# Optimization experiments

Hardware: AMD Instinct MI355X
Metric: run time of the kernel (lower is better)

Reference implementation:

```python
import jax, jax.numpy as jnp
import numpy as np

DIM = 4096
N_HEADS = 32
N_KV_HEADS = 8
HEAD_DIM = DIM // N_HEADS            # 128
GROUP = N_HEADS // N_KV_HEADS        # 4 heads share each kv head


def setup_inputs() -> dict:
    key = jax.random.key(0)
    k1, k2, k3, k4 = jax.random.split(key, 4)
    B, S = 2, 2048
    x = jax.random.normal(k1, (B, S, DIM), dtype=jnp.float32)
    # nn.Linear weights are [out_features, in_features]
    Wq = jax.random.normal(k2, (N_HEADS * HEAD_DIM, DIM), dtype=jnp.float32) * 0.02
    Wkv = jax.random.normal(k3, (2 * N_KV_HEADS * HEAD_DIM, DIM), dtype=jnp.float32) * 0.02
    Wo = jax.random.normal(k4, (DIM, N_HEADS * HEAD_DIM), dtype=jnp.float32) * 0.02
    return {"x": x, "Wq": Wq, "Wkv": Wkv, "Wo": Wo, "start_pos": 0}


def reference(x, Wq, Wkv, Wo, start_pos):
    B, S, _ = x.shape
    total_len = start_pos + S
    # projections (Linear: x @ W.T)
    q = (x @ Wq.T).reshape(B, S, N_HEADS, HEAD_DIM)                  # (B,S,H,D)
    kv = (x @ Wkv.T).reshape(B, S, 2 * N_KV_HEADS, HEAD_DIM)
    k, v = jnp.split(kv, 2, axis=2)                                   # (B,S,Hkv,D) each
    # cache write + read with start_pos=0 is identity on k, v (prefill)
    # inflate kv heads: repeat_interleave along head axis
    k = jnp.repeat(k, GROUP, axis=2)                                  # (B,T,H,D)
    v = jnp.repeat(v, GROUP, axis=2)
    scale = HEAD_DIM ** -0.5
    scores = jnp.einsum('bqhd,bkhd->bhqk', q, k) * scale              # (B,H,S,T)
    q_idx = jnp.arange(total_len - S, total_len)[:, None]
    k_idx = jnp.arange(total_len)[None, :]
    causal = q_idx >= k_idx                                           # (S,T)
    scores = jnp.where(causal[None, None], scores, -jnp.inf)
    probs = jax.nn.softmax(scores, axis=-1)
    attn = jnp.einsum('bhqk,bkhd->bqhd', probs, v)                    # (B,S,H,D)
    attn = attn.reshape(B, S, N_HEADS * HEAD_DIM)
    return attn @ Wo.T                                                # (B,S,dim)
```

## Files before the change

kernel.cpp:

```cpp
#include <hip/hip_runtime.h>

typedef __bf16 bf16x8 __attribute__((ext_vector_type(8)));
typedef __bf16 bf16x4 __attribute__((ext_vector_type(4)));
typedef float f32x4 __attribute__((ext_vector_type(4)));
typedef unsigned short u16;
typedef unsigned short u16x8 __attribute__((ext_vector_type(8)));

#define DIM 4096
#define NHEADS 32
#define NKV 8
#define HD 128
#define BB 2
#define SS 2048
#define MROWS (BB*SS)
#define QKVP 6144
#define QSCALE 0.08838834764831843f

#define WAIT_LGKM0 asm volatile("s_waitcnt lgkmcnt(0)" ::: "memory")
#define WAIT_VM0   asm volatile("s_waitcnt vmcnt(0)" ::: "memory")
#define WAIT_VM4   asm volatile("s_waitcnt vmcnt(4)" ::: "memory")
#define WAIT_VM8   asm volatile("s_waitcnt vmcnt(8)" ::: "memory")
#define SGB0       __builtin_amdgcn_sched_barrier(0)

__device__ __forceinline__ u16 f2bf(float f) {
  unsigned int u = __float_as_uint(f);
  u += 0x7fffu + ((u >> 16) & 1u);
  return (u16)(u >> 16);
}

__device__ __forceinline__ void gload16(const void* g, void* l) {
  __builtin_amdgcn_global_load_lds(
      (const __attribute__((address_space(1))) unsigned int*)g,
      (__attribute__((address_space(3))) unsigned int*)l, 16, 0, 0);
}

__device__ __forceinline__ bf16x4 tr16(const void* p) {
  bf16x4 d;
  asm volatile("ds_read_b64_tr_b16 %0, %1"
               : "=v"(d)
               : "v"((const __attribute__((address_space(3))) u16*)p)
               : "memory");
  return d;
}

template<int CTRL>
__device__ __forceinline__ float dpp_ror(float x) {
  return __int_as_float(__builtin_amdgcn_update_dpp(
      0, __float_as_int(x), CTRL, 0xF, 0xF, false));
}
__device__ __forceinline__ float red16_max(float v) {
  v = fmaxf(v, dpp_ror<0x121>(v));
  v = fmaxf(v, dpp_ror<0x122>(v));
  v = fmaxf(v, dpp_ror<0x124>(v));
  v = fmaxf(v, dpp_ror<0x128>(v));
  return v;
}
__device__ __forceinline__ float red16_sum(float v) {
  v += dpp_ror<0x121>(v);
  v += dpp_ror<0x122>(v);
  v += dpp_ror<0x124>(v);
  v += dpp_ror<0x128>(v);
  return v;
}

__global__ __launch_bounds__(256) void f2b_kernel(const float* __restrict__ in,
                                                  u16* __restrict__ out, int n8) {
  int i = blockIdx.x * 256 + threadIdx.x;
  if (i >= n8) return;
  const float4* in4 = (const float4*)in;
  float4 a = in4[2*(size_t)i];
  float4 b = in4[2*(size_t)i + 1];
  u16x8 o;
  o[0]=f2bf(a.x); o[1]=f2bf(a.y); o[2]=f2bf(a.z); o[3]=f2bf(a.w);
  o[4]=f2bf(b.x); o[5]=f2bf(b.y); o[6]=f2bf(b.z); o[7]=f2bf(b.w);
  ((u16x8*)out)[i] = o;
}

template<int OUTF32>
__global__ __launch_bounds__(512, 2) void gemm256(
    const u16* __restrict__ A, const u16* __restrict__ Bm, void* __restrict__ C,
    int M, int N, int K, int nbx, int acut, float a0, float a1) {
  __shared__ char smem[131072];

  const int t = threadIdx.x;
  const int l = t & 63, w = t >> 6;
  const int l15 = l & 15, l4 = l >> 4;
  const int wm = w >> 2, wn = w & 3;

  const int nwg = gridDim.x;
  const int cpx = nwg >> 3;
  const int sw = (blockIdx.x & 7) * cpx + (blockIdx.x >> 3);
  const int bx = sw % nbx, by = sw / nbx;
  const int row0 = by * 256, col0 = bx * 256;
  const float alpha = (col0 < acut) ? a0 : a1;

  f32x4 acc[8][4] = {};

  auto stage = [&](int kt) {
    const int bsel = kt & 3;
    const int k0 = kt << 5;
    char* Ad = smem + bsel * 16384;
    char* Bd = smem + 65536 + bsel * 16384;
    #pragma unroll
    for (int i = 0; i < 2; ++i) {
      int o = (i*8 + w)*64 + l;
      int j = o >> 3;
      int cs = (o & 7) ^ (j & 7);
      int r = 2*j + (cs >> 2);
      int kc = (cs & 3) * 8;
      gload16((const char*)A + ((size_t)(row0 + r)*K + k0 + kc)*2,
              Ad + (i*8 + w)*1024);
      gload16((const char*)Bm + ((size_t)(col0 + r)*K + k0 + kc)*2,
              Bd + (i*8 + w)*1024);
    }
  };

  const int nt = K >> 5;
  stage(0); stage(1); stage(2);
  WAIT_VM8;
  __builtin_amdgcn_s_barrier();
  SGB0;

  for (int kt = 0; kt < nt; ++kt) {
    if (kt + 3 < nt) { stage(kt + 3); WAIT_VM8; }
    else if (kt + 2 < nt) { WAIT_VM4; }
    else if (kt + 1 < nt) { WAIT_VM0; }
    __builtin_amdgcn_s_barrier();
    SGB0;

    const char* Ab = smem + (kt & 3) * 16384;
    const char* Bb = smem + 65536 + (kt & 3) * 16384;
    bf16x8 af[8], bfv[4];
    #pragma unroll
    for (int mi = 0; mi < 8; ++mi) {
      int r = wm*128 + mi*16 + l15;
      int j = r >> 1;
      int c = ((r & 1)*4 + l4) ^ (j & 7);
      af[mi] = *(const bf16x8*)(Ab + j*128 + c*16);
    }
    #pragma unroll
    for (int ni = 0; ni < 4; ++ni) {
      int r = wn*64 + ni*16 + l15;
      int j = r >> 1;
      int c = ((r & 1)*4 + l4) ^ (j & 7);
      bfv[ni] = *(const bf16x8*)(Bb + j*128 + c*16);
    }
    __builtin_amdgcn_s_setprio(1);
    #pragma unroll
    for (int mi = 0; mi < 8; ++mi)
      #pragma unroll
      for (int ni = 0; ni < 4; ++ni)
        acc[mi][ni] = __builtin_amdgcn_mfma_f32_16x16x32_bf16(
            af[mi], bfv[ni], acc[mi][ni], 0, 0, 0);
    __builtin_amdgcn_s_setprio(0);
    SGB0;
    __builtin_amdgcn_s_barrier();
    SGB0;
  }

  #pragma unroll
  for (int mi = 0; mi < 8; ++mi) {
    #pragma unroll
    for (int ni = 0; ni < 4; ++ni) {
      #pragma unroll
      for (int r = 0; r < 4; ++r) {
        size_t rr = (size_t)(row0 + wm*128 + mi*16 + l4*4 + r);
        size_t cc = (size_t)(col0 + wn*64 + ni*16 + l15);
        float v = acc[mi][ni][r] * alpha;
        if (OUTF32) ((float*)C)[rr*(size_t)N + cc] = v;
        else        ((u16*)C)[rr*(size_t)N + cc] = f2bf(v);
      }
    }
  }
}

__global__ __launch_bounds__(256, 2) void attn_kernel(
    const u16* __restrict__ QKV,
    u16* __restrict__ O) {
  __shared__ u16 Ks[2][64*128];
  __shared__ u16 Vs[2][64*128];
  __shared__ u16 Ps[4][1024];
  const int t = threadIdx.x;
  const int l = t & 63, w = t >> 6;
  const int l15 = l & 15, l4 = l >> 4;
  const int pair = blockIdx.x, h = blockIdx.y, b = blockIdx.z;
  const int hkv = h >> 2;
  const u16* Kg = QKV + (size_t)(b*SS) * QKVP + DIM + hkv*HD;
  const u16* Vg = Kg + NKV*HD;
  u16* Pw = &Ps[w][0];

  auto stage = [&](u16* Ksb, u16* Vsb, int kv0) {
    const u16* Kr = Kg + (size_t)kv0 * QKVP;
    const u16* Vr = Vg + (size_t)kv0 * QKVP;
    #pragma unroll
    for (int i = 0; i < 4; ++i) {
      int o = i*4096 + w*1024 + l*16;
      int row = o >> 8;
      int sc = l15 ^ (row & 7);
      gload16((const char*)(Kr + (size_t)row * QKVP) + sc*16,
              (char*)Ksb + i*4096 + w*1024);
    }
    #pragma unroll
    for (int i = 0; i < 4; ++i) {
      int cb = i*4 + w;
      int kv = cb*4 + ((l & 7) >> 1);
      int d0 = ((l >> 3) << 4) + (l & 1)*8;
      gload16((const char*)(Vr + (size_t)kv * QKVP + d0),
              (char*)Vsb + cb*1024);
    }
  };

  for (int half = 0; half < 2; ++half) {
    const int qb = half ? (15 - pair) : pair;
    const int q0 = qb * 128;
    const int q0w = q0 + w*32;

    const size_t qbase = ((size_t)(b*SS + q0w)) * QKVP + h*HD;
    bf16x8 qf[2][4];
    #pragma unroll
    for (int m = 0; m < 2; ++m)
      #pragma unroll
      for (int kd = 0; kd < 4; ++kd)
        qf[m][kd] = *(const bf16x8*)&QKV[qbase + (size_t)(m*16 + l15)*QKVP + kd*32 + l4*8];

    f32x4 oacc[2][8] = {};
    float mrun[2][4], lrun[2][4];
    #pragma unroll
    for (int m = 0; m < 2; ++m)
      #pragma unroll
      for (int r = 0; r < 4; ++r) { mrun[m][r] = -1e30f; lrun[m][r] = 0.f; }

    const int nst = 2*qb + 2;
    stage(Ks[0], Vs[0], 0);
    WAIT_VM0;
    __builtin_amdgcn_s_barrier();
    SGB0;

    for (int st = 0; st < nst; ++st) {
      const int kv0 = st * 64;
      u16* Ksb = Ks[st & 1];
      u16* Vsb = Vs[st & 1];
      if (st + 1 < nst) stage(Ks[(st+1) & 1], Vs[(st+1) & 1], kv0 + 64);

      if (kv0 <= q0w + 31) {
        f32x4 sacc[2][4] = {};
        __builtin_amdgcn_s_setprio(1);
        #pragma unroll
        for (int kd = 0; kd < 4; ++kd) {
          bf16x8 kf[4];
          #pragma unroll
          for (int n = 0; n < 4; ++n) {
            int row = n*16 + l15;
            int off = (row << 8) | (((kd*4 + l4) ^ (row & 7)) << 4);
            kf[n] = *(const bf16x8*)((const char*)Ksb + off);
          }
          #pragma unroll
          for (int m = 0; m < 2; ++m)
            #pragma unroll
            for (int n = 0; n < 4; ++n)
              sacc[m][n] = __builtin_amdgcn_mfma_f32_16x16x32_bf16(qf[m][kd], kf[n], sacc[m][n], 0, 0, 0);
        }
        __builtin_amdgcn_s_setprio(0);

        if (st >= 2*qb) {
          #pragma unroll
          for (int n = 0; n < 4; ++n) {
            int ki = kv0 + n*16 + l15;
            #pragma unroll
            for (int m = 0; m < 2; ++m)
              #pragma unroll
              for (int r = 0; r < 4; ++r) {
                int qi = q0w + m*16 + l4*4 + r;
                if (ki > qi) sacc[m][n][r] = -1e30f;
              }
          }
        }

        float pr[2][4][4];
        #pragma unroll
        for (int m = 0; m < 2; ++m) {
          #pragma unroll
          for (int r = 0; r < 4; ++r) {
            float s0 = sacc[m][0][r], s1 = sacc[m][1][r];
            float s2 = sacc[m][2][r], s3 = sacc[m][3][r];
            float vm = fmaxf(fmaxf(s0, s1), fmaxf(s2, s3));
            vm = red16_max(vm);
            float mo = mrun[m][r];
            float mnew = fmaxf(mo, vm);
            float al = __expf(mo - mnew);
            float p0 = __expf(s0 - mnew), p1 = __expf(s1 - mnew);
            float p2 = __expf(s2 - mnew), p3 = __expf(s3 - mnew);
            float rs = red16_sum((p0 + p1) + (p2 + p3));
            mrun[m][r] = mnew;
            lrun[m][r] = lrun[m][r]*al + rs;
            #pragma unroll
            for (int dn = 0; dn < 8; ++dn) oacc[m][dn][r] *= al;
            pr[m][r][0] = p0; pr[m][r][1] = p1; pr[m][r][2] = p2; pr[m][r][3] = p3;
          }
        }

        #pragma unroll
        for (int kvh = 0; kvh < 2; ++kvh) {
          #pragma unroll
          for (int m = 0; m < 2; ++m)
            #pragma unroll
            for (int nn = 0; nn < 2; ++nn) {
              int n = kvh*2 + nn;
              bf16x4 w4;
              w4[0] = (__bf16)pr[m][0][n]; w4[1] = (__bf16)pr[m][1][n];
              w4[2] = (__bf16)pr[m][2][n]; w4[3] = (__bf16)pr[m][3][n];
              *(bf16x4*)((char*)Pw + ((nn*4 + (l15 >> 2))*2 + m)*128
                                   + (l15 & 3)*32 + l4*8) = w4;
            }
          const char* pb = (const char*)Pw + l4*512 + l15*8;
          bf16x4 a00 = tr16(pb);
          bf16x4 a01 = tr16(pb + 256);
          bf16x4 a10 = tr16(pb + 128);
          bf16x4 a11 = tr16(pb + 384);
          const char* vb = (const char*)Vsb + l4*2048 + l15*8 + kvh*8192;
          bf16x4 b0[8], b1[8];
          #pragma unroll
          for (int dn = 0; dn < 8; ++dn) {
            b0[dn] = tr16(vb + dn*128);
            b1[dn] = tr16(vb + dn*128 + 1024);
          }
          WAIT_LGKM0; SGB0;
          bf16x8 pa0 = __builtin_shufflevector(a00, a01, 0,1,2,3,4,5,6,7);
          bf16x8 pa1 = __builtin_shufflevector(a10, a11, 0,1,2,3,4,5,6,7);
          __builtin_amdgcn_s_setprio(1);
          #pragma unroll
          for (int dn = 0; dn < 8; ++dn) {
            bf16x8 v8 = __builtin_shufflevector(b0[dn], b1[dn], 0,1,2,3,4,5,6,7);
            oacc[0][dn] = __builtin_amdgcn_mfma_f32_16x16x32_bf16(pa0, v8, oacc[0][dn], 0, 0, 0);
            oacc[1][dn] = __builtin_amdgcn_mfma_f32_16x16x32_bf16(pa1, v8, oacc[1][dn], 0, 0, 0);
          }
          __builtin_amdgcn_s_setprio(0);
        }
      }

      WAIT_VM0;
      __builtin_amdgcn_s_barrier();
      SGB0;
    }

    const size_t obase = ((size_t)(b*SS + q0w)) * DIM + h*HD;
    #pragma unroll
    for (int m = 0; m < 2; ++m) {
      #pragma unroll
      for (int r = 0; r < 4; ++r) {
        float inv = 1.0f / lrun[m][r];
        int srow = m*16 + l4*4 + r;
        #pragma unroll
        for (int dn = 0; dn < 8; ++dn)
          O[obase + (size_t)srow*DIM + dn*16 + l15] = f2bf(oacc[m][dn][r] * inv);
      }
    }
  }
}

extern "C" void kernel_launch(void* const* d_in, const int* in_sizes, int n_in,
                              void* d_out, int out_size, void* d_ws, size_t ws_size,
                              hipStream_t stream) {
  const float* x   = (const float*)d_in[0];
  const float* Wq  = (const float*)d_in[1];
  const float* Wkv = (const float*)d_in[2];
  const float* Wo  = (const float*)d_in[3];

  if (ws_size < (160ull << 20)) return;
  char* ws = (char*)d_ws;
  u16* xb   = (u16*)(ws);
  u16* Wqb  = (u16*)(ws + (32ull  << 20));
  u16* Wkvb = (u16*)(ws + (64ull  << 20));
  u16* Wob  = (u16*)(ws + (80ull  << 20));
  u16* QKVb = (u16*)(ws + (112ull << 20));
  u16* attnb = xb;

  f2b_kernel<<<8192, 256, 0, stream>>>(x,   xb,   2097152);
  f2b_kernel<<<8192, 256, 0, stream>>>(Wq,  Wqb,  2097152);
  f2b_kernel<<<4096, 256, 0, stream>>>(Wkv, Wkvb, 1048576);
  f2b_kernel<<<8192, 256, 0, stream>>>(Wo,  Wob,  2097152);

  gemm256<0><<<dim3(16*24), 512, 0, stream>>>(xb, Wqb, QKVb,
                                              MROWS, QKVP, DIM, 24, DIM, QSCALE, 1.0f);

  attn_kernel<<<dim3(8, NHEADS, BB), 256, 0, stream>>>(QKVb, attnb);

  gemm256<1><<<dim3(16*16), 512, 0, stream>>>(attnb, Wob, d_out,
                                              MROWS, DIM, DIM, 16, 0, 1.0f, 1.0f);
}
```

Before: 571.4 us.

## Split GEMM main loop into two MFMA phases interleaved with A/B prefetch

Restructures the bf16 GEMM K-loop so each iteration runs two halves of MFMAs (rows 0-3, then 4-7). The global prefetch of the A tile is issued during the first half and the B tile during the second, with barriers and priority hints between them. The vmcnt wait moves to the end of the iteration so loads for the next tile overlap compute. The aim is to hide global-load and LDS-read latency behind MFMA work and to lower fragment register pressure. The cost is extra barriers per iteration, which could add synchronization stalls.

```diff
diff --git a/kernel.cpp b/kernel.cpp
--- a/kernel.cpp
+++ b/kernel.cpp
@@ -96,11 +96,10 @@
 
   f32x4 acc[8][4] = {};
 
-  auto stage = [&](int kt) {
+  auto stageM = [&](const u16* Mp, int base0, int kt) {
     const int bsel = kt & 3;
     const int k0 = kt << 5;
-    char* Ad = smem + bsel * 16384;
-    char* Bd = smem + 65536 + bsel * 16384;
+    char* Md = smem + base0 + bsel * 16384;
     #pragma unroll
     for (int i = 0; i < 2; ++i) {
       int o = (i*8 + w)*64 + l;
@@ -108,54 +107,89 @@
       int cs = (o & 7) ^ (j & 7);
       int r = 2*j + (cs >> 2);
       int kc = (cs & 3) * 8;
-      gload16((const char*)A + ((size_t)(row0 + r)*K + k0 + kc)*2,
-              Ad + (i*8 + w)*1024);
-      gload16((const char*)Bm + ((size_t)(col0 + r)*K + k0 + kc)*2,
-              Bd + (i*8 + w)*1024);
+      gload16((const char*)Mp + ((size_t)(base0 ? col0 + r : row0 + r)*K + k0 + kc)*2,
+              Md + (i*8 + w)*1024);
     }
   };
 
+  auto ldA = [&](const char* Ab, int mi) -> bf16x8 {
+    int r = wm*128 + mi*16 + l15;
+    int j = r >> 1;
+    int c = ((r & 1)*4 + l4) ^ (j & 7);
+    return *(const bf16x8*)(Ab + j*128 + c*16);
+  };
+  auto ldB = [&](const char* Bb, int ni) -> bf16x8 {
+    int r = wn*64 + ni*16 + l15;
+    int j = r >> 1;
+    int c = ((r & 1)*4 + l4) ^ (j & 7);
+    return *(const bf16x8*)(Bb + j*128 + c*16);
+  };
+
   const int nt = K >> 5;
-  stage(0); stage(1); stage(2);
+  stageM(A, 0, 0); stageM(Bm, 65536, 0);
+  stageM(A, 0, 1); stageM(Bm, 65536, 1);
+  stageM(A, 0, 2); stageM(Bm, 65536, 2);
   WAIT_VM8;
   __builtin_amdgcn_s_barrier();
-  SGB0;
 
   for (int kt = 0; kt < nt; ++kt) {
-    if (kt + 3 < nt) { stage(kt + 3); WAIT_VM8; }
-    else if (kt + 2 < nt) { WAIT_VM4; }
-    else if (kt + 1 < nt) { WAIT_VM0; }
-    __builtin_amdgcn_s_barrier();
-    SGB0;
-
     const char* Ab = smem + (kt & 3) * 16384;
     const char* Bb = smem + 65536 + (kt & 3) * 16384;
-    bf16x8 af[8], bfv[4];
-    #pragma unroll
-    for (int mi = 0; mi < 8; ++mi) {
-      int r = wm*128 + mi*16 + l15;
-      int j = r >> 1;
-      int c = ((r & 1)*4 + l4) ^ (j & 7);
-      af[mi] = *(const bf16x8*)(Ab + j*128 + c*16);
-    }
-    #pragma unroll
-    for (int ni = 0; ni < 4; ++ni) {
-      int r = wn*64 + ni*16 + l15;
-      int j = r >> 1;
-      int c = ((r & 1)*4 + l4) ^ (j & 7);
-      bfv[ni] = *(const bf16x8*)(Bb + j*128 + c*16);
-    }
+    const bool pf = (kt + 3 < nt);
+
+    bf16x8 af0 = ldA(Ab, 0), af1 = ldA(Ab, 1), af2 = ldA(Ab, 2), af3 = ldA(Ab, 3);
+    bf16x8 bf0 = ldB(Bb, 0), bf1 = ldB(Bb, 1), bf2 = ldB(Bb, 2), bf3 = ldB(Bb, 3);
+    SGB0;
+    if (pf) stageM(A, 0, kt + 3);
+    __builtin_amdgcn_s_barrier();
+    WAIT_LGKM0; SGB0;
     __builtin_amdgcn_s_setprio(1);
-    #pragma unroll
-    for (int mi = 0; mi < 8; ++mi)
-      #pragma unroll
-      for (int ni = 0; ni < 4; ++ni)
-        acc[mi][ni] = __builtin_amdgcn_mfma_f32_16x16x32_bf16(
-            af[mi], bfv[ni], acc[mi][ni], 0, 0, 0);
+    acc[0][0] = __builtin_amdgcn_mfma_f32_16x16x32_bf16(af0, bf0, acc[0][0], 0, 0, 0);
+    acc[0][1] = __builtin_amdgcn_mfma_f32_16x16x32_bf16(af0, bf1, acc[0][1], 0, 0, 0);
+    acc[0][2] = __builtin_amdgcn_mfma_f32_16x16x32_bf16(af0, bf2, acc[0][2], 0, 0, 0);
+    acc[0][3] = __builtin_amdgcn_mfma_f32_16x16x32_bf16(af0, bf3, acc[0][3], 0, 0, 0);
+    acc[1][0] = __builtin_amdgcn_mfma_f32_16x16x32_bf16(af1, bf0, acc[1][0], 0, 0, 0);
+    acc[1][1] = __builtin_amdgcn_mfma_f32_16x16x32_bf16(af1, bf1, acc[1][1], 0, 0, 0);
+    acc[1][2] = __builtin_amdgcn_mfma_f32_16x16x32_bf16(af1, bf2, acc[1][2], 0, 0, 0);
+    acc[1][3] = __builtin_amdgcn_mfma_f32_16x16x32_bf16(af1, bf3, acc[1][3], 0, 0, 0);
+    acc[2][0] = __builtin_amdgcn_mfma_f32_16x16x32_bf16(af2, bf0, acc[2][0], 0, 0, 0);
+    acc[2][1] = __builtin_amdgcn_mfma_f32_16x16x32_bf16(af2, bf1, acc[2][1], 0, 0, 0);
+    acc[2][2] = __builtin_amdgcn_mfma_f32_16x16x32_bf16(af2, bf2, acc[2][2], 0, 0, 0);
+    acc[2][3] = __builtin_amdgcn_mfma_f32_16x16x32_bf16(af2, bf3, acc[2][3], 0, 0, 0);
+    acc[3][0] = __builtin_amdgcn_mfma_f32_16x16x32_bf16(af3, bf0, acc[3][0], 0, 0, 0);
+    acc[3][1] = __builtin_amdgcn_mfma_f32_16x16x32_bf16(af3, bf1, acc[3][1], 0, 0, 0);
+    acc[3][2] = __builtin_amdgcn_mfma_f32_16x16x32_bf16(af3, bf2, acc[3][2], 0, 0, 0);
+    acc[3][3] = __builtin_amdgcn_mfma_f32_16x16x32_bf16(af3, bf3, acc[3][3], 0, 0, 0);
     __builtin_amdgcn_s_setprio(0);
+    __builtin_amdgcn_s_barrier();
+
+    bf16x8 af4 = ldA(Ab, 4), af5 = ldA(Ab, 5), af6 = ldA(Ab, 6), af7 = ldA(Ab, 7);
     SGB0;
+    if (pf) stageM(Bm, 65536, kt + 3);
     __builtin_amdgcn_s_barrier();
-    SGB0;
+    WAIT_LGKM0; SGB0;
+    __builtin_amdgcn_s_setprio(1);
+    acc[4][0] = __builtin_amdgcn_mfma_f32_16x16x32_bf16(af4, bf0, acc[4][0], 0, 0, 0);
+    acc[4][1] = __builtin_amdgcn_mfma_f32_16x16x32_bf16(af4, bf1, acc[4][1], 0, 0, 0);
+    acc[4][2] = __builtin_amdgcn_mfma_f32_16x16x32_bf16(af4, bf2, acc[4][2], 0, 0, 0);
+    acc[4][3] = __builtin_amdgcn_mfma_f32_16x16x32_bf16(af4, bf3, acc[4][3], 0, 0, 0);
+    acc[5][0] = __builtin_amdgcn_mfma_f32_16x16x32_bf16(af5, bf0, acc[5][0], 0, 0, 0);
+    acc[5][1] = __builtin_amdgcn_mfma_f32_16x16x32_bf16(af5, bf1, acc[5][1], 0, 0, 0);
+    acc[5][2] = __builtin_amdgcn_mfma_f32_16x16x32_bf16(af5, bf2, acc[5][2], 0, 0, 0);
+    acc[5][3] = __builtin_amdgcn_mfma_f32_16x16x32_bf16(af5, bf3, acc[5][3], 0, 0, 0);
+    acc[6][0] = __builtin_amdgcn_mfma_f32_16x16x32_bf16(af6, bf0, acc[6][0], 0, 0, 0);
+    acc[6][1] = __builtin_amdgcn_mfma_f32_16x16x32_bf16(af6, bf1, acc[6][1], 0, 0, 0);
+    acc[6][2] = __builtin_amdgcn_mfma_f32_16x16x32_bf16(af6, bf2, acc[6][2], 0, 0, 0);
+    acc[6][3] = __builtin_amdgcn_mfma_f32_16x16x32_bf16(af6, bf3, acc[6][3], 0, 0, 0);
+    acc[7][0] = __builtin_amdgcn_mfma_f32_16x16x32_bf16(af7, bf0, acc[7][0], 0, 0, 0);
+    acc[7][1] = __builtin_amdgcn_mfma_f32_16x16x32_bf16(af7, bf1, acc[7][1], 0, 0, 0);
+    acc[7][2] = __builtin_amdgcn_mfma_f32_16x16x32_bf16(af7, bf2, acc[7][2], 0, 0, 0);
+    acc[7][3] = __builtin_amdgcn_mfma_f32_16x16x32_bf16(af7, bf3, acc[7][3], 0, 0, 0);
+    __builtin_amdgcn_s_setprio(0);
+    if (pf)                { WAIT_VM8; }
+    else if (kt + 2 < nt)  { WAIT_VM4; }
+    else if (kt + 1 < nt)  { WAIT_VM0; }
+    __builtin_amdgcn_s_barrier();
   }
 
   #pragma unroll
```

Result: no change. 564.5 us (-1.2%).

## Software-pipeline GEMM LDS fragment loads and merge four conversion kernels

Applied to the files above, without the earlier changes.

The GEMM main loop is unrolled by two with ping-pong register fragment sets. Each iteration issues the LDS reads for the next k-tile while the MFMAs for the current tile run, and keeps one barrier per tile instead of two. Global load addresses are precomputed once and advanced by pointer increments, which removes the per-stage index math. The four fp32-to-bf16 conversion launches are merged into a single launch. The risks are higher register pressure from holding two fragment sets and a tighter WAR margin on the four-buffer LDS ring.

```diff
diff --git a/kernel.cpp b/kernel.cpp
--- a/kernel.cpp
+++ b/kernel.cpp
@@ -19,7 +19,6 @@
 #define WAIT_LGKM0 asm volatile("s_waitcnt lgkmcnt(0)" ::: "memory")
 #define WAIT_VM0   asm volatile("s_waitcnt vmcnt(0)" ::: "memory")
 #define WAIT_VM4   asm volatile("s_waitcnt vmcnt(4)" ::: "memory")
-#define WAIT_VM8   asm volatile("s_waitcnt vmcnt(8)" ::: "memory")
 #define SGB0       __builtin_amdgcn_sched_barrier(0)
 
 __device__ __forceinline__ u16 f2bf(float f) {
@@ -63,17 +62,24 @@
   return v;
 }
 
-__global__ __launch_bounds__(256) void f2b_kernel(const float* __restrict__ in,
-                                                  u16* __restrict__ out, int n8) {
+__global__ __launch_bounds__(256) void f2b4_kernel(
+    const float* __restrict__ xa, const float* __restrict__ xb,
+    const float* __restrict__ xc, const float* __restrict__ xd,
+    u16* __restrict__ oa, u16* __restrict__ ob,
+    u16* __restrict__ oc, u16* __restrict__ od) {
   int i = blockIdx.x * 256 + threadIdx.x;
-  if (i >= n8) return;
+  const float* in; u16* out; int k;
+  if (i < 2097152)      { in = xa; out = oa; k = i; }
+  else if (i < 4194304) { in = xb; out = ob; k = i - 2097152; }
+  else if (i < 5242880) { in = xc; out = oc; k = i - 4194304; }
+  else                  { in = xd; out = od; k = i - 5242880; }
   const float4* in4 = (const float4*)in;
-  float4 a = in4[2*(size_t)i];
-  float4 b = in4[2*(size_t)i + 1];
+  float4 a = in4[2*(size_t)k];
+  float4 b = in4[2*(size_t)k + 1];
   u16x8 o;
   o[0]=f2bf(a.x); o[1]=f2bf(a.y); o[2]=f2bf(a.z); o[3]=f2bf(a.w);
   o[4]=f2bf(b.x); o[5]=f2bf(b.y); o[6]=f2bf(b.z); o[7]=f2bf(b.w);
-  ((u16x8*)out)[i] = o;
+  ((u16x8*)out)[k] = o;
 }
 
 template<int OUTF32>
@@ -96,66 +102,127 @@
 
   f32x4 acc[8][4] = {};
 
-  auto stage = [&](int kt) {
-    const int bsel = kt & 3;
-    const int k0 = kt << 5;
-    char* Ad = smem + bsel * 16384;
-    char* Bd = smem + 65536 + bsel * 16384;
-    #pragma unroll
-    for (int i = 0; i < 2; ++i) {
-      int o = (i*8 + w)*64 + l;
-      int j = o >> 3;
-      int cs = (o & 7) ^ (j & 7);
-      int r = 2*j + (cs >> 2);
-      int kc = (cs & 3) * 8;
-      gload16((const char*)A + ((size_t)(row0 + r)*K + k0 + kc)*2,
-              Ad + (i*8 + w)*1024);
-      gload16((const char*)Bm + ((size_t)(col0 + r)*K + k0 + kc)*2,
-              Bd + (i*8 + w)*1024);
-    }
+  int ro0, ko0, ro1, ko1;
+  {
+    int o = t, j = o >> 3, cs = (o & 7) ^ (j & 7);
+    ro0 = 2*j + (cs >> 2); ko0 = (cs & 3) * 8;
+    o = t + 512; j = o >> 3; cs = (o & 7) ^ (j & 7);
+    ro1 = 2*j + (cs >> 2); ko1 = (cs & 3) * 8;
+  }
+  const char* gA0 = (const char*)(A  + (size_t)(row0 + ro0) * K + ko0);
+  const char* gA1 = (const char*)(A  + (size_t)(row0 + ro1) * K + ko1);
+  const char* gB0 = (const char*)(Bm + (size_t)(col0 + ro0) * K + ko0);
+  const char* gB1 = (const char*)(Bm + (size_t)(col0 + ro1) * K + ko1);
+
+  auto stage = [&](int bsel) {
+    char* Ad = (char*)smem + bsel * 16384;
+    char* Bd = Ad + 65536;
+    gload16(gA0, Ad + w*1024);
+    gload16(gA1, Ad + 8192 + w*1024);
+    gload16(gB0, Bd + w*1024);
+    gload16(gB1, Bd + 8192 + w*1024);
+    gA0 += 64; gA1 += 64; gB0 += 64; gB1 += 64;
   };
 
+  int offA0, offB0;
+  {
+    int r = wm*128 + l15, j = r >> 1;
+    int c = ((r & 1)*4 + l4) ^ (j & 7);
+    offA0 = j*128 + c*16;
+    r = wn*64 + l15; j = r >> 1;
+    c = ((r & 1)*4 + l4) ^ (j & 7);
+    offB0 = 65536 + j*128 + c*16;
+  }
+
+  struct Frags { bf16x8 a0,a1,a2,a3,a4,a5,a6,a7,b0,b1,b2,b3; };
+  Frags F0, F1;
+
+  auto loadF = [&](Frags& F, int bsel) {
+    const char* Sb = (const char*)smem + bsel * 16384;
+    const char* Ab = Sb + offA0;
+    const char* Bb = Sb + offB0;
+    F.a0 = *(const bf16x8*)(Ab);
+    F.a1 = *(const bf16x8*)(Ab + 1024);
+    F.a2 = *(const bf16x8*)(Ab + 2048);
+    F.a3 = *(const bf16x8*)(Ab + 3072);
+    F.a4 = *(const bf16x8*)(Ab + 4096);
+    F.a5 = *(const bf16x8*)(Ab + 5120);
+    F.a6 = *(const bf16x8*)(Ab + 6144);
+    F.a7 = *(const bf16x8*)(Ab + 7168);
+    F.b0 = *(const bf16x8*)(Bb);
+    F.b1 = *(const bf16x8*)(Bb + 1024);
+    F.b2 = *(const bf16x8*)(Bb + 2048);
+    F.b3 = *(const bf16x8*)(Bb + 3072);
+  };
+
+  auto mfmaC = [&](const Frags& F) {
+    __builtin_amdgcn_s_setprio(1);
+    acc[0][0] = __builtin_amdgcn_mfma_f32_16x16x32_bf16(F.a0, F.b0, acc[0][0], 0, 0, 0);
+    acc[0][1] = __builtin_amdgcn_mfma_f32_16x16x32_bf16(F.a0, F.b1, acc[0][1], 0, 0, 0);
+    acc[0][2] = __builtin_amdgcn_mfma_f32_16x16x32_bf16(F.a0, F.b2, acc[0][2], 0, 0, 0);
+    acc[0][3] = __builtin_amdgcn_mfma_f32_16x16x32_bf16(F.a0, F.b3, acc[0][3], 0, 0, 0);
+    acc[1][0] = __builtin_amdgcn_mfma_f32_16x16x32_bf16(F.a1, F.b0, acc[1][0], 0, 0, 0);
+    acc[1][1] = __builtin_amdgcn_mfma_f32_16x16x32_bf16(F.a1, F.b1, acc[1][1], 0, 0, 0);
+    acc[1][2] = __builtin_amdgcn_mfma_f32_16x16x32_bf16(F.a1, F.b2, acc[1][2], 0, 0, 0);
+    acc[1][3] = __builtin_amdgcn_mfma_f32_16x16x32_bf16(F.a1, F.b3, acc[1][3], 0, 0, 0);
+    acc[2][0] = __builtin_amdgcn_mfma_f32_16x16x32_bf16(F.a2, F.b0, acc[2][0], 0, 0, 0);
+    acc[2][1] = __builtin_amdgcn_mfma_f32_16x16x32_bf16(F.a2, F.b1, acc[2][1], 0, 0, 0);
+    acc[2][2] = __builtin_amdgcn_mfma_f32_16x16x32_bf16(F.a2, F.b2, acc[2][2], 0, 0, 0);
+    acc[2][3] = __builtin_amdgcn_mfma_f32_16x16x32_bf16(F.a2, F.b3, acc[2][3], 0, 0, 0);
+    acc[3][0] = __builtin_amdgcn_mfma_f32_16x16x32_bf16(F.a3, F.b0, acc[3][0], 0, 0, 0);
+    acc[3][1] = __builtin_amdgcn_mfma_f32_16x16x32_bf16(F.a3, F.b1, acc[3][1], 0, 0, 0);
+    acc[3][2] = __builtin_amdgcn_mfma_f32_16x16x32_bf16(F.a3, F.b2, acc[3][2], 0, 0, 0);
+    acc[3][3] = __builtin_amdgcn_mfma_f32_16x16x32_bf16(F.a3, F.b3, acc[3][3], 0, 0, 0);
+    acc[4][0] = __builtin_amdgcn_mfma_f32_16x16x32_bf16(F.a4, F.b0, acc[4][0], 0, 0, 0);
+    acc[4][1] = __builtin_amdgcn_mfma_f32_16x16x32_bf16(F.a4, F.b1, acc[4][1], 0, 0, 0);
+    acc[4][2] = __builtin_amdgcn_mfma_f32_16x16x32_bf16(F.a4, F.b2, acc[4][2], 0, 0, 0);
+    acc[4][3] = __builtin_amdgcn_mfma_f32_16x16x32_bf16(F.a4, F.b3, acc[4][3], 0, 0, 0);
+    acc[5][0] = __builtin_amdgcn_mfma_f32_16x16x32_bf16(F.a5, F.b0, acc[5][0], 0, 0, 0);
+    acc[5][1] = __builtin_amdgcn_mfma_f32_16x16x32_bf16(F.a5, F.b1, acc[5][1], 0, 0, 0);
+    acc[5][2] = __builtin_amdgcn_mfma_f32_16x16x32_bf16(F.a5, F.b2, acc[5][2], 0, 0, 0);
+    acc[5][3] = __builtin_amdgcn_mfma_f32_16x16x32_bf16(F.a5, F.b3, acc[5][3], 0, 0, 0);
+    acc[6][0] = __builtin_amdgcn_mfma_f32_16x16x32_bf16(F.a6, F.b0, acc[6][0], 0, 0, 0);
+    acc[6][1] = __builtin_amdgcn_mfma_f32_16x16x32_bf16(F.a6, F.b1, acc[6][1], 0, 0, 0);
+    acc[6][2] = __builtin_amdgcn_mfma_f32_16x16x32_bf16(F.a6, F.b2, acc[6][2], 0, 0, 0);
+    acc[6][3] = __builtin_amdgcn_mfma_f32_16x16x32_bf16(F.a6, F.b3, acc[6][3], 0, 0, 0);
+    acc[7][0] = __builtin_amdgcn_mfma_f32_16x16x32_bf16(F.a7, F.b0, acc[7][0], 0, 0, 0);
+    acc[7][1] = __builtin_amdgcn_mfma_f32_16x16x32_bf16(F.a7, F.b1, acc[7][1], 0, 0, 0);
+    acc[7][2] = __builtin_amdgcn_mfma_f32_16x16x32_bf16(F.a7, F.b2, acc[7][2], 0, 0, 0);
+    acc[7][3] = __builtin_amdgcn_mfma_f32_16x16x32_bf16(F.a7, F.b3, acc[7][3], 0, 0, 0);
+    __builtin_amdgcn_s_setprio(0);
+  };
+
   const int nt = K >> 5;
+
   stage(0); stage(1); stage(2);
-  WAIT_VM8;
+  WAIT_VM4;
   __builtin_amdgcn_s_barrier();
-  SGB0;
-
-  for (int kt = 0; kt < nt; ++kt) {
-    if (kt + 3 < nt) { stage(kt + 3); WAIT_VM8; }
-    else if (kt + 2 < nt) { WAIT_VM4; }
-    else if (kt + 1 < nt) { WAIT_VM0; }
-    __builtin_amdgcn_s_barrier();
-    SGB0;
-
-    const char* Ab = smem + (kt & 3) * 16384;
-    const char* Bb = smem + 65536 + (kt & 3) * 16384;
-    bf16x8 af[8], bfv[4];
-    #pragma unroll
-    for (int mi = 0; mi < 8; ++mi) {
-      int r = wm*128 + mi*16 + l15;
-      int j = r >> 1;
-      int c = ((r & 1)*4 + l4) ^ (j & 7);
-      af[mi] = *(const bf16x8*)(Ab + j*128 + c*16);
-    }
-    #pragma unroll
-    for (int ni = 0; ni < 4; ++ni) {
-      int r = wn*64 + ni*16 + l15;
-      int j = r >> 1;
-      int c = ((r & 1)*4 + l4) ^ (j & 7);
-      bfv[ni] = *(const bf16x8*)(Bb + j*128 + c*16);
-    }
-    __builtin_amdgcn_s_setprio(1);
-    #pragma unroll
-    for (int mi = 0; mi < 8; ++mi)
-      #pragma unroll
-      for (int ni = 0; ni < 4; ++ni)
-        acc[mi][ni] = __builtin_amdgcn_mfma_f32_16x16x32_bf16(
-            af[mi], bfv[ni], acc[mi][ni], 0, 0, 0);
-    __builtin_amdgcn_s_setprio(0);
-    SGB0;
-    __builtin_amdgcn_s_barrier();
-    SGB0;
+  loadF(F0, 0);
+  WAIT_LGKM0; SGB0;
+
+  for (int i = 0; i < nt; i += 2) {
+    {
+      const bool pf = (i + 3 < nt);
+      if (pf) stage((i + 3) & 3);
+      if (i + 1 < nt) loadF(F1, (i + 1) & 3);
+      SGB0;
+      mfmaC(F0);
+      SGB0;
+      WAIT_LGKM0; SGB0;
+      if (pf) { WAIT_VM4; } else { WAIT_VM0; }
+      __builtin_amdgcn_s_barrier();
+    }
+    if (i + 1 < nt) {
+      const bool pf = (i + 4 < nt);
+      if (pf) stage((i + 4) & 3);
+      if (i + 2 < nt) loadF(F0, (i + 2) & 3);
+      SGB0;
+      mfmaC(F1);
+      SGB0;
+      WAIT_LGKM0; SGB0;
+      if (pf) { WAIT_VM4; } else { WAIT_VM0; }
+      __builtin_amdgcn_s_barrier();
+    }
   }
 
   #pragma unroll
@@ -375,10 +442,7 @@
   u16* QKVb = (u16*)(ws + (112ull << 20));
   u16* attnb = xb;
 
-  f2b_kernel<<<8192, 256, 0, stream>>>(x,   xb,   2097152);
-  f2b_kernel<<<8192, 256, 0, stream>>>(Wq,  Wqb,  2097152);
-  f2b_kernel<<<4096, 256, 0, stream>>>(Wkv, Wkvb, 1048576);
-  f2b_kernel<<<8192, 256, 0, stream>>>(Wo,  Wob,  2097152);
+  f2b4_kernel<<<28672, 256, 0, stream>>>(x, Wq, Wkv, Wo, xb, Wqb, Wkvb, Wob);
 
   gemm256<0><<<dim3(16*24), 512, 0, stream>>>(xb, Wqb, QKVb,
                                               MROWS, QKVP, DIM, 24, DIM, QSCALE, 1.0f);
```

New measurement: 543.6 us. -4.9%, faster.

## Load GEMM B operand directly to registers and fuse the four bf16 conversion launches

Applied to the files above, without the earlier changes.

The GEMM mainloop now stages only the A tile through LDS, double-buffered with a K-step of 64, and reads the B operand straight from global memory into registers. This halves LDS use and removes the LDS reads for B, but each wave now issues its own B global loads and the pipeline is shallower (2 buffers instead of 4). The four fp32-to-bf16 conversion launches are also merged into one kernel that picks its source by index range, cutting launch overhead.

```diff
diff --git a/kernel.cpp b/kernel.cpp
--- a/kernel.cpp
+++ b/kernel.cpp
@@ -63,24 +63,31 @@
   return v;
 }
 
-__global__ __launch_bounds__(256) void f2b_kernel(const float* __restrict__ in,
-                                                  u16* __restrict__ out, int n8) {
+__global__ __launch_bounds__(256) void f2b4_kernel(
+    const float* __restrict__ xa, const float* __restrict__ xb,
+    const float* __restrict__ xc, const float* __restrict__ xd,
+    u16* __restrict__ oa, u16* __restrict__ ob,
+    u16* __restrict__ oc, u16* __restrict__ od) {
   int i = blockIdx.x * 256 + threadIdx.x;
-  if (i >= n8) return;
+  const float* in; u16* out; int k;
+  if (i < 2097152)      { in = xa; out = oa; k = i; }
+  else if (i < 4194304) { in = xb; out = ob; k = i - 2097152; }
+  else if (i < 5242880) { in = xc; out = oc; k = i - 4194304; }
+  else                  { in = xd; out = od; k = i - 5242880; }
   const float4* in4 = (const float4*)in;
-  float4 a = in4[2*(size_t)i];
-  float4 b = in4[2*(size_t)i + 1];
+  float4 a = in4[2*(size_t)k];
+  float4 b = in4[2*(size_t)k + 1];
   u16x8 o;
   o[0]=f2bf(a.x); o[1]=f2bf(a.y); o[2]=f2bf(a.z); o[3]=f2bf(a.w);
   o[4]=f2bf(b.x); o[5]=f2bf(b.y); o[6]=f2bf(b.z); o[7]=f2bf(b.w);
-  ((u16x8*)out)[i] = o;
+  ((u16x8*)out)[k] = o;
 }
 
 template<int OUTF32>
 __global__ __launch_bounds__(512, 2) void gemm256(
     const u16* __restrict__ A, const u16* __restrict__ Bm, void* __restrict__ C,
     int M, int N, int K, int nbx, int acut, float a0, float a1) {
-  __shared__ char smem[131072];
+  __shared__ char smem[65536];
 
   const int t = threadIdx.x;
   const int l = t & 63, w = t >> 6;
@@ -96,67 +103,81 @@
 
   f32x4 acc[8][4] = {};
 
-  auto stage = [&](int kt) {
-    const int bsel = kt & 3;
-    const int k0 = kt << 5;
-    char* Ad = smem + bsel * 16384;
-    char* Bd = smem + 65536 + bsel * 16384;
-    #pragma unroll
-    for (int i = 0; i < 2; ++i) {
-      int o = (i*8 + w)*64 + l;
-      int j = o >> 3;
-      int cs = (o & 7) ^ (j & 7);
-      int r = 2*j + (cs >> 2);
-      int kc = (cs & 3) * 8;
-      gload16((const char*)A + ((size_t)(row0 + r)*K + k0 + kc)*2,
-              Ad + (i*8 + w)*1024);
-      gload16((const char*)Bm + ((size_t)(col0 + r)*K + k0 + kc)*2,
-              Bd + (i*8 + w)*1024);
-    }
+  const int jrow = w*8 + (l >> 3);
+  const int csw  = (l & 7) ^ (l >> 3);
+  const u16* pA = A + (size_t)(row0 + jrow) * K + csw * 8;
+  char* const ldsw = (char*)smem + w*1024;
+
+  auto stageA = [&](int tile) {
+    const u16* s = pA + tile * 64;
+    char* d = ldsw + (tile & 1) * 32768;
+    gload16(s,                  d);
+    gload16(s + (size_t)64*K,   d + 8192);
+    gload16(s + (size_t)128*K,  d + 16384);
+    gload16(s + (size_t)192*K,  d + 24576);
   };
 
-  const int nt = K >> 5;
-  stage(0); stage(1); stage(2);
-  WAIT_VM8;
+  const u16* pB = Bm + (size_t)(col0 + wn*64 + l15) * K + l4 * 8;
+  const size_t bstride = (size_t)16 * K;
+
+  bf16x8 Ar[8][2], Br[4][2];
+
+  auto loadB = [&](int tile) {
+    const u16* s = pB + tile * 64;
+    #pragma unroll
+    for (int ni = 0; ni < 4; ++ni) {
+      Br[ni][0] = *(const bf16x8*)(s + (size_t)ni * bstride);
+      Br[ni][1] = *(const bf16x8*)(s + (size_t)ni * bstride + 32);
+    }
+  };
+
+  const int cxk0 = ((0*4 + l4) ^ (l15 & 7)) * 16;
+  const int cxk1 = ((1*4 + l4) ^ (l15 & 7)) * 16;
+  const int abase = wm*16384 + l15*128;
+
+  auto rdA = [&](int dbuf) {
+    const char* Ab = (const char*)smem + dbuf*32768 + abase;
+    #pragma unroll
+    for (int mi = 0; mi < 8; ++mi) {
+      Ar[mi][0] = *(const bf16x8*)(Ab + mi*2048 + cxk0);
+      Ar[mi][1] = *(const bf16x8*)(Ab + mi*2048 + cxk1);
+    }
+  };
+
+  auto mfma64 = [&]() {
+    __builtin_amdgcn_s_setprio(1);
+    #pragma unroll
+    for (int kk = 0; kk < 2; ++kk)
+      #pragma unroll
+      for (int mi = 0; mi < 8; ++mi)
+        #pragma unroll
+        for (int ni = 0; ni < 4; ++ni)
+          acc[mi][ni] = __builtin_amdgcn_mfma_f32_16x16x32_bf16(
+              Ar[mi][kk], Br[ni][kk], acc[mi][ni], 0, 0, 0);
+    __builtin_amdgcn_s_setprio(0);
+  };
+
+  const int nt = K >> 6;
+
+  stageA(0);
+  loadB(0);
+  WAIT_VM0;
   __builtin_amdgcn_s_barrier();
-  SGB0;
-
-  for (int kt = 0; kt < nt; ++kt) {
-    if (kt + 3 < nt) { stage(kt + 3); WAIT_VM8; }
-    else if (kt + 2 < nt) { WAIT_VM4; }
-    else if (kt + 1 < nt) { WAIT_VM0; }
+
+  for (int i = 0; i < nt - 1; ++i) {
+    rdA(i & 1);
+    stageA(i + 1);
+    WAIT_VM4;
+    WAIT_LGKM0; SGB0;
+    mfma64();
+    loadB(i + 1);
+    WAIT_VM8;
     __builtin_amdgcn_s_barrier();
-    SGB0;
-
-    const char* Ab = smem + (kt & 3) * 16384;
-    const char* Bb = smem + 65536 + (kt & 3) * 16384;
-    bf16x8 af[8], bfv[4];
-    #pragma unroll
-    for (int mi = 0; mi < 8; ++mi) {
-      int r = wm*128 + mi*16 + l15;
-      int j = r >> 1;
-      int c = ((r & 1)*4 + l4) ^ (j & 7);
-      af[mi] = *(const bf16x8*)(Ab + j*128 + c*16);
-    }
-    #pragma unroll
-    for (int ni = 0; ni < 4; ++ni) {
-      int r = wn*64 + ni*16 + l15;
-      int j = r >> 1;
-      int c = ((r & 1)*4 + l4) ^ (j & 7);
-      bfv[ni] = *(const bf16x8*)(Bb + j*128 + c*16);
-    }
-    __builtin_amdgcn_s_setprio(1);
-    #pragma unroll
-    for (int mi = 0; mi < 8; ++mi)
-      #pragma unroll
-      for (int ni = 0; ni < 4; ++ni)
-        acc[mi][ni] = __builtin_amdgcn_mfma_f32_16x16x32_bf16(
-            af[mi], bfv[ni], acc[mi][ni], 0, 0, 0);
-    __builtin_amdgcn_s_setprio(0);
-    SGB0;
-    __builtin_amdgcn_s_barrier();
-    SGB0;
   }
+  rdA((nt - 1) & 1);
+  WAIT_VM0;
+  WAIT_LGKM0; SGB0;
+  mfma64();
 
   #pragma unroll
   for (int mi = 0; mi < 8; ++mi) {
@@ -375,10 +396,7 @@
   u16* QKVb = (u16*)(ws + (112ull << 20));
   u16* attnb = xb;
 
-  f2b_kernel<<<8192, 256, 0, stream>>>(x,   xb,   2097152);
-  f2b_kernel<<<8192, 256, 0, stream>>>(Wq,  Wqb,  2097152);
-  f2b_kernel<<<4096, 256, 0, stream>>>(Wkv, Wkvb, 1048576);
-  f2b_kernel<<<8192, 256, 0, stream>>>(Wo,  Wob,  2097152);
+  f2b4_kernel<<<28672, 256, 0, stream>>>(x, Wq, Wkv, Wo, xb, Wqb, Wkvb, Wob);
 
   gemm256<0><<<dim3(16*24), 512, 0, stream>>>(xb, Wqb, QKVb,
                                               MROWS, QKVP, DIM, 24, DIM, QSCALE, 1.0f);
```

Result: slower. 691.9 us (+21.1%).
